# Kernel tuning notes

Hardware: AMD Instinct MI355X
Metric: run time of the kernel (lower is better)

Reference implementation:

```python
import jax, jax.numpy as jnp
import numpy as np

N_NODES = 100000


def gcn_conv(x, W, b, src, dst, n):
    # x: [N, Fin], W: [Fin, Fout]. GCNConv: D^-1/2 (A+I) D^-1/2 (X W) + b
    h = x @ W  # [N, Fout]
    ones = jnp.ones_like(dst, dtype=h.dtype)
    deg = jax.ops.segment_sum(ones, dst, num_segments=n)  # in-degree incl self-loops
    dinv = jnp.where(deg > 0, jax.lax.rsqrt(deg), 0.0)
    norm = dinv[src] * dinv[dst]  # [E]
    msg = h[src] * norm[:, None]  # gather + scale
    out = jax.ops.segment_sum(msg, dst, num_segments=n)  # scatter-add
    return out + b


def setup_inputs() -> dict:
    key = jax.random.key(0)
    k1, k2, k3, k4 = jax.random.split(key, 4)
    F_IN, H, C, E = 512, 256, 40, 3200000
    x = jax.random.normal(k1, (N_NODES, F_IN), dtype=jnp.float32)
    # glorot-ish init
    W1 = jax.random.normal(k2, (F_IN, H), dtype=jnp.float32) * (1.0 / np.sqrt(F_IN))
    b1 = jnp.zeros((H,), dtype=jnp.float32)
    W2 = jax.random.normal(k3, (H, C), dtype=jnp.float32) * (1.0 / np.sqrt(H))
    b2 = jnp.zeros((C,), dtype=jnp.float32)
    edge_index = jax.random.randint(k4, (2, E), 0, N_NODES, dtype=jnp.int64)
    return {"x": x, "W1": W1, "b1": b1, "W2": W2, "b2": b2, "edge_index": edge_index}


def reference(x, W1, b1, W2, b2, edge_index):
    n = x.shape[0]
    # add self-loops (PyG GCNConv default add_self_loops=True)
    loop = jnp.arange(n, dtype=edge_index.dtype)
    src = jnp.concatenate([edge_index[0], loop])
    dst = jnp.concatenate([edge_index[1], loop])
    h = gcn_conv(x, W1, b1, src, dst, n)
    h = jax.nn.relu(h)
    # F.dropout(training=self.training): identity in eval mode
    h = gcn_conv(h, W2, b2, src, dst, n)
    return jax.nn.log_softmax(h, axis=1)
```

## Files before the change

kernel.cpp:

```cpp
#include <hip/hip_runtime.h>
#include <stdint.h>

typedef __attribute__((ext_vector_type(8))) short bf16x8;
typedef __attribute__((ext_vector_type(4))) float f32x4;
typedef __attribute__((ext_vector_type(4))) int i32x4;

__device__ __forceinline__ unsigned short f2bf(float f) {
    unsigned int u = __float_as_uint(f);
    u += 0x7FFFu + ((u >> 16) & 1u);
    return (unsigned short)(u >> 16);
}
__device__ __forceinline__ float bf2f(unsigned short s) {
    return __uint_as_float(((unsigned int)s) << 16);
}
__device__ __forceinline__ unsigned char fp8_enc(float f) {
    f = fminf(fmaxf(f, -448.f), 448.f);
    unsigned int u = __float_as_uint(f * 0x1p-120f);
    u += 0x7FFFFu + ((u >> 20) & 1u);
    return (unsigned char)(((u >> 20) & 0x7F) | ((u >> 24) & 0x80));
}

#define SLAB_CAP 5120

__global__ __launch_bounds__(256) void k_bscatter(const int* __restrict__ src,
                                                  const int* __restrict__ dst, int E,
                                                  int* __restrict__ bcnt,
                                                  int* __restrict__ slab, int nbuck) {
    __shared__ int lh[1024];
    __shared__ int lcur[1024];
    const int CH = 8192;
    int e0 = blockIdx.x * CH;
    int e1 = min(E, e0 + CH);
    for (int i = threadIdx.x; i < nbuck; i += 256) lh[i] = 0;
    __syncthreads();
    for (int i = e0 + threadIdx.x; i < e1; i += 256) atomicAdd(&lh[dst[i] >> 7], 1);
    __syncthreads();
    for (int i = threadIdx.x; i < nbuck; i += 256) {
        int c = lh[i];
        lh[i] = c ? atomicAdd(&bcnt[i], c) : 0;
        lcur[i] = 0;
    }
    __syncthreads();
    for (int i = e0 + threadIdx.x; i < e1; i += 256) {
        int d = dst[i], s = src[i];
        int b = d >> 7;
        int p = lh[b] + atomicAdd(&lcur[b], 1);
        if (p < SLAB_CAP) slab[(size_t)b * SLAB_CAP + p] = ((d & 127) << 20) | s;
    }
}

__global__ __launch_bounds__(1024) void k_bscan(const int* __restrict__ bcnt,
                                                int* __restrict__ bbase, int nbuck) {
    __shared__ int sh[1024];
    int t = threadIdx.x;
    int v = (t < nbuck) ? min(bcnt[t], SLAB_CAP) : 0;
    sh[t] = v;
    __syncthreads();
    for (int off = 1; off < 1024; off <<= 1) {
        int x = (t >= off) ? sh[t - off] : 0;
        __syncthreads();
        sh[t] += x;
        __syncthreads();
    }
    if (t < nbuck) bbase[t] = sh[t] - v;
    if (t == 1023) bbase[nbuck] = sh[1023];
}

__global__ __launch_bounds__(256) void k_bcsr(const int* __restrict__ slab,
                                              const int* __restrict__ bcnt,
                                              const int* __restrict__ bbase,
                                              int* __restrict__ rowp,
                                              int* __restrict__ col,
                                              float* __restrict__ dinv, int n, int nbuck) {
    __shared__ int lh[128], lsc[128], lcur[128];
    const int b = blockIdx.x;
    const int base = bbase[b];
    const int cnt = min(bcnt[b], SLAB_CAP);
    const int t = threadIdx.x;
    const int* sl = slab + (size_t)b * SLAB_CAP;
    if (t < 128) lh[t] = 0;
    __syncthreads();
    for (int i = t; i < cnt; i += 256) atomicAdd(&lh[sl[i] >> 20], 1);
    __syncthreads();
    if (t < 128) lsc[t] = lh[t];
    __syncthreads();
    for (int off = 1; off < 128; off <<= 1) {
        int x = (t < 128 && t >= off) ? lsc[t - off] : 0;
        __syncthreads();
        if (t < 128) lsc[t] += x;
        __syncthreads();
    }
    if (t < 128) {
        int excl = lsc[t] - lh[t];
        lcur[t] = excl;
        int v = (b << 7) + t;
        if (v < n) {
            rowp[v] = base + excl;
            dinv[v] = rsqrtf((float)lh[t] + 1.0f);
        }
    }
    if (b == 0 && t == 0) rowp[n] = bbase[nbuck];
    __syncthreads();
    for (int i = t; i < cnt; i += 256) {
        int pk = sl[i];
        int d = pk >> 20;
        int p = base + atomicAdd(&lcur[d], 1);
        col[p] = pk & 0xFFFFF;
    }
}

__global__ __launch_bounds__(256) void k_cvt_w(const float* __restrict__ W1,
                                               const float* __restrict__ W2,
                                               short* __restrict__ W1t,
                                               short* __restrict__ W2t,
                                               int n1, int n2) {
    int i = blockIdx.x * blockDim.x + threadIdx.x;
    if (i < n1) {
        int k = i >> 8, c = i & 255;
        W1t[(size_t)c * 512 + k] = (short)f2bf(W1[i]);
    } else if (i < n1 + n2) {
        int i2 = i - n1;
        int k = i2 / 40, c = i2 - k * 40;
        W2t[(size_t)c * 256 + k] = (short)f2bf(W2[i2]);
    }
}

__global__ __launch_bounds__(512) void k_gemm1(const float* __restrict__ A,
                                               const short* __restrict__ Bt,
                                               const float* __restrict__ dinv,
                                               unsigned char* __restrict__ outp, int M) {
    const int K = 512;
    __shared__ __align__(16) short As[128 * 32];
    __shared__ __align__(16) short Bs[256 * 32];
    const int tid = threadIdx.x;
    const int m0 = blockIdx.x * 128;
    const int w = tid >> 6, lane = tid & 63;
    const int quad = lane >> 4, l16 = lane & 15;
    const int mbase = (w >> 2) * 64, nbase = (w & 3) * 64;

    f32x4 acc[4][4];
#pragma unroll
    for (int i = 0; i < 4; i++)
#pragma unroll
        for (int j = 0; j < 4; j++) acc[i][j] = (f32x4){0.f, 0.f, 0.f, 0.f};

    for (int k0 = 0; k0 < K; k0 += 32) {
#pragma unroll
        for (int s = tid; s < 1024; s += 512) {
            int r = s >> 3, seg = s & 7;
            int gr = m0 + r;
            if (gr >= M) gr = M - 1;
            float4 v = *(const float4*)(A + (size_t)gr * K + k0 + seg * 4);
            ushort4 o;
            o.x = f2bf(v.x); o.y = f2bf(v.y); o.z = f2bf(v.z); o.w = f2bf(v.w);
            *(ushort4*)(As + r * 32 + seg * 4) = o;
        }
#pragma unroll
        for (int s = tid; s < 1024; s += 512) {
            int r = s >> 2, seg = s & 3;
            i32x4 v = *(const i32x4*)(Bt + (size_t)r * K + k0 + seg * 8);
            *(i32x4*)(Bs + r * 32 + seg * 8) = v;
        }
        __syncthreads();
        bf16x8 af[4], bfr[4];
#pragma unroll
        for (int i = 0; i < 4; i++)
            af[i] = *(const bf16x8*)(As + (mbase + i * 16 + l16) * 32 + quad * 8);
#pragma unroll
        for (int j = 0; j < 4; j++)
            bfr[j] = *(const bf16x8*)(Bs + (nbase + j * 16 + l16) * 32 + quad * 8);
#pragma unroll
        for (int i = 0; i < 4; i++)
#pragma unroll
            for (int j = 0; j < 4; j++)
                acc[i][j] = __builtin_amdgcn_mfma_f32_16x16x32_bf16(af[i], bfr[j], acc[i][j], 0, 0, 0);
        __syncthreads();
    }

#pragma unroll
    for (int i = 0; i < 4; i++) {
#pragma unroll
        for (int r = 0; r < 4; r++) {
            int row = m0 + mbase + i * 16 + quad * 4 + r;
            if (row < M) {
                float dv = dinv[row] * 64.f;
#pragma unroll
                for (int j = 0; j < 4; j++)
                    outp[(size_t)row * 256 + nbase + j * 16 + l16] =
                        fp8_enc(acc[i][j][r] * dv);
            }
        }
    }
}

template <int NJ>
__global__ __launch_bounds__(256) void k_gemm_bt(const short* __restrict__ A,
                                                 const short* __restrict__ Bt,
                                                 const float* __restrict__ dinv,
                                                 short* __restrict__ outp,
                                                 int M, int K, int ldo, int ncols) {
    constexpr int BN = 32 * NJ;
    __shared__ __align__(16) short As[128 * 32];
    __shared__ __align__(16) short Bs[BN * 32];
    const int tid = threadIdx.x;
    const int m0 = blockIdx.x * 128;
    const int n0 = blockIdx.y * BN;
    const int w = tid >> 6, lane = tid & 63;
    const int quad = lane >> 4, l16 = lane & 15;
    const int mbase = (w >> 1) * 64, nbase = (w & 1) * (NJ * 16);

    f32x4 acc[4][NJ];
#pragma unroll
    for (int i = 0; i < 4; i++)
#pragma unroll
        for (int j = 0; j < NJ; j++) acc[i][j] = (f32x4){0.f, 0.f, 0.f, 0.f};

    for (int k0 = 0; k0 < K; k0 += 32) {
#pragma unroll
        for (int s = tid; s < 512; s += 256) {
            int r = s >> 2, seg = s & 3;
            int gr = m0 + r;
            if (gr >= M) gr = M - 1;
            i32x4 v = *(const i32x4*)(A + (size_t)gr * K + k0 + seg * 8);
            *(i32x4*)(As + r * 32 + seg * 8) = v;
        }
#pragma unroll
        for (int s = tid; s < BN * 4; s += 256) {
            int r = s >> 2, seg = s & 3;
            i32x4 v = *(const i32x4*)(Bt + (size_t)(n0 + r) * K + k0 + seg * 8);
            *(i32x4*)(Bs + r * 32 + seg * 8) = v;
        }
        __syncthreads();
        bf16x8 af[4], bfr[NJ];
#pragma unroll
        for (int i = 0; i < 4; i++)
            af[i] = *(const bf16x8*)(As + (mbase + i * 16 + l16) * 32 + quad * 8);
#pragma unroll
        for (int j = 0; j < NJ; j++)
            bfr[j] = *(const bf16x8*)(Bs + (nbase + j * 16 + l16) * 32 + quad * 8);
#pragma unroll
        for (int i = 0; i < 4; i++)
#pragma unroll
            for (int j = 0; j < NJ; j++)
                acc[i][j] = __builtin_amdgcn_mfma_f32_16x16x32_bf16(af[i], bfr[j], acc[i][j], 0, 0, 0);
        __syncthreads();
    }

#pragma unroll
    for (int i = 0; i < 4; i++) {
#pragma unroll
        for (int r = 0; r < 4; r++) {
            int row = m0 + mbase + i * 16 + quad * 4 + r;
            if (row < M) {
                float dv = dinv[row];
#pragma unroll
                for (int j = 0; j < NJ; j++) {
                    int c = n0 + nbase + j * 16 + l16;
                    if (c < ncols)
                        outp[(size_t)row * ldo + c] = (short)f2bf(acc[i][j][r] * dv);
                }
            }
        }
    }
}

__global__ __launch_bounds__(256) void k_agg1(const unsigned char* __restrict__ h1p,
                                              const int* __restrict__ rowp,
                                              const int* __restrict__ col,
                                              const float* __restrict__ dinv,
                                              const float* __restrict__ b1,
                                              short* __restrict__ h2, int n) {
    const unsigned int* __restrict__ hw = (const unsigned int*)h1p;
    const int w = threadIdx.x >> 6, lane = threadIdx.x & 63;
    const int v = blockIdx.x * 4 + w;
    if (v >= n) return;
    float a0, a1, a2, a3;
    {
        unsigned int u = hw[(size_t)v * 64 + lane];
        a0 = __builtin_amdgcn_cvt_f32_fp8(u, 0);
        a1 = __builtin_amdgcn_cvt_f32_fp8(u, 1);
        a2 = __builtin_amdgcn_cvt_f32_fp8(u, 2);
        a3 = __builtin_amdgcn_cvt_f32_fp8(u, 3);
    }
    const int e0 = rowp[v], e1 = rowp[v + 1];
    int e = e0;
    for (; e + 4 <= e1; e += 4) {
        int s0 = col[e], s1 = col[e + 1], s2 = col[e + 2], s3 = col[e + 3];
        unsigned int u0 = hw[(size_t)s0 * 64 + lane];
        unsigned int u1 = hw[(size_t)s1 * 64 + lane];
        unsigned int u2 = hw[(size_t)s2 * 64 + lane];
        unsigned int u3 = hw[(size_t)s3 * 64 + lane];
        a0 += __builtin_amdgcn_cvt_f32_fp8(u0, 0) + __builtin_amdgcn_cvt_f32_fp8(u1, 0)
            + __builtin_amdgcn_cvt_f32_fp8(u2, 0) + __builtin_amdgcn_cvt_f32_fp8(u3, 0);
        a1 += __builtin_amdgcn_cvt_f32_fp8(u0, 1) + __builtin_amdgcn_cvt_f32_fp8(u1, 1)
            + __builtin_amdgcn_cvt_f32_fp8(u2, 1) + __builtin_amdgcn_cvt_f32_fp8(u3, 1);
        a2 += __builtin_amdgcn_cvt_f32_fp8(u0, 2) + __builtin_amdgcn_cvt_f32_fp8(u1, 2)
            + __builtin_amdgcn_cvt_f32_fp8(u2, 2) + __builtin_amdgcn_cvt_f32_fp8(u3, 2);
        a3 += __builtin_amdgcn_cvt_f32_fp8(u0, 3) + __builtin_amdgcn_cvt_f32_fp8(u1, 3)
            + __builtin_amdgcn_cvt_f32_fp8(u2, 3) + __builtin_amdgcn_cvt_f32_fp8(u3, 3);
    }
    for (; e < e1; e++) {
        unsigned int u = hw[(size_t)col[e] * 64 + lane];
        a0 += __builtin_amdgcn_cvt_f32_fp8(u, 0);
        a1 += __builtin_amdgcn_cvt_f32_fp8(u, 1);
        a2 += __builtin_amdgcn_cvt_f32_fp8(u, 2);
        a3 += __builtin_amdgcn_cvt_f32_fp8(u, 3);
    }
    const int c4 = lane * 4;
    const float dv = dinv[v] * 0x1p-6f;
    float r0 = fmaxf(fmaf(dv, a0, b1[c4 + 0]), 0.f);
    float r1 = fmaxf(fmaf(dv, a1, b1[c4 + 1]), 0.f);
    float r2 = fmaxf(fmaf(dv, a2, b1[c4 + 2]), 0.f);
    float r3 = fmaxf(fmaf(dv, a3, b1[c4 + 3]), 0.f);
    ushort4 o;
    o.x = f2bf(r0); o.y = f2bf(r1); o.z = f2bf(r2); o.w = f2bf(r3);
    *(ushort4*)(h2 + (size_t)v * 256 + c4) = o;
}

__global__ __launch_bounds__(256) void k_agg2(const short* __restrict__ zp,
                                              const int* __restrict__ rowp,
                                              const int* __restrict__ col,
                                              const float* __restrict__ dinv,
                                              const float* __restrict__ b2,
                                              float* __restrict__ out, int n) {
    const int w = threadIdx.x >> 6, lane = threadIdx.x & 63;
    const int v = blockIdx.x * 4 + w;
    if (v >= n) return;
    const bool act = lane < 40;
    const int li = act ? lane : 0;
    float acc = act ? bf2f((unsigned short)zp[(size_t)v * 40 + li]) : 0.f;
    const int e0 = rowp[v], e1 = rowp[v + 1];
    int e = e0;
    for (; e + 4 <= e1; e += 4) {
        int sa = col[e], sb = col[e + 1], sc = col[e + 2], sd = col[e + 3];
        float fa = bf2f((unsigned short)zp[(size_t)sa * 40 + li]);
        float fb = bf2f((unsigned short)zp[(size_t)sb * 40 + li]);
        float fc = bf2f((unsigned short)zp[(size_t)sc * 40 + li]);
        float fd = bf2f((unsigned short)zp[(size_t)sd * 40 + li]);
        if (act) acc += fa + fb + fc + fd;
    }
    for (; e < e1; e++) {
        float f = bf2f((unsigned short)zp[(size_t)col[e] * 40 + li]);
        if (act) acc += f;
    }
    float logit = act ? fmaf(dinv[v], acc, b2[li]) : -1e30f;
    float m = logit;
    for (int off = 32; off; off >>= 1) m = fmaxf(m, __shfl_xor(m, off));
    float ex = act ? expf(logit - m) : 0.f;
    float ssum = ex;
    for (int off = 32; off; off >>= 1) ssum += __shfl_xor(ssum, off);
    if (act) out[(size_t)v * 40 + lane] = logit - m - logf(ssum);
}

extern "C" void kernel_launch(void* const* d_in, const int* in_sizes, int n_in,
                              void* d_out, int out_size, void* d_ws, size_t ws_size,
                              hipStream_t stream) {
    const float* x  = (const float*)d_in[0];
    const float* W1 = (const float*)d_in[1];
    const float* b1 = (const float*)d_in[2];
    const float* W2 = (const float*)d_in[3];
    const float* b2 = (const float*)d_in[4];
    const int*   ei = (const int*)d_in[5];
    float* out = (float*)d_out;

    const int FIN = 512, H = 256, C = 40;
    const int n = in_sizes[0] / FIN;
    const int E = in_sizes[5] / 2;
    const int nbuck = (n + 127) >> 7;

    auto align_up = [](size_t v) { return (v + 255) & ~(size_t)255; };
    char* base = (char*)d_ws;
    size_t off = 0;
    unsigned char* h1p = (unsigned char*)(base + off); off += align_up((size_t)n * H);
    short* h2    = (short*)(base + off); off += align_up((size_t)n * H * 2);
    short* zp    = (short*)(base + off); off += align_up((size_t)n * C * 2);
    float* dinv  = (float*)(base + off); off += align_up((size_t)n * 4);
    int* rowp    = (int*)(base + off);   off += align_up((size_t)(n + 1) * 4);
    int* colarr  = (int*)(base + off);   off += align_up((size_t)E * 4);
    int* slab    = (int*)(base + off);   off += align_up((size_t)nbuck * SLAB_CAP * 4);
    short* W1t   = (short*)(base + off); off += align_up((size_t)H * FIN * 2);
    short* W2t   = (short*)(base + off); off += align_up((size_t)64 * H * 2);
    int* bcnt    = (int*)(base + off);   off += align_up((size_t)(nbuck + 1) * 4);
    int* bbase   = (int*)(base + off);   off += align_up((size_t)(nbuck + 1) * 4);

    const int* srcp = ei;
    const int* dstp = ei + E;

    hipMemsetAsync(bcnt, 0, (size_t)(nbuck + 1) * 4, stream);
    hipMemsetAsync(W2t, 0, (size_t)64 * H * 2, stream);

    k_bscatter<<<(E + 8191) / 8192, 256, 0, stream>>>(srcp, dstp, E, bcnt, slab, nbuck);
    k_bscan<<<1, 1024, 0, stream>>>(bcnt, bbase, nbuck);
    k_bcsr<<<nbuck, 256, 0, stream>>>(slab, bcnt, bbase, rowp, colarr, dinv, n, nbuck);

    int n1 = FIN * H, n2 = H * C;
    k_cvt_w<<<(n1 + n2 + 255) / 256, 256, 0, stream>>>(W1, W2, W1t, W2t, n1, n2);

    k_gemm1<<<(n + 127) / 128, 512, 0, stream>>>(x, W1t, dinv, h1p, n);
    k_agg1<<<(n + 3) / 4, 256, 0, stream>>>(h1p, rowp, colarr, dinv, b1, h2, n);

    dim3 g2((n + 127) / 128, 1);
    k_gemm_bt<2><<<g2, 256, 0, stream>>>(h2, W2t, dinv, zp, n, H, C, C);
    k_agg2<<<(n + 3) / 4, 256, 0, stream>>>(zp, rowp, colarr, dinv, b2, out, n);
}
```

Baseline: 702.2 us.

## Store layer-2 features as scaled fp8 and aggregate four nodes per wavefront

The second GEMM now writes dinv-scaled features as fp8 (times 64) in a 64-byte padded row instead of 40 bf16 values. The layer-2 aggregation reads them as 32-bit words. Each 16-lane group handles one node with four features per lane, so a wavefront covers four nodes instead of one node with 24 idle lanes. This targets the cost of the random gather in the second aggregation and the wasted lanes, at the price of lower precision in the layer-2 messages.

```diff
diff --git a/kernel.cpp b/kernel.cpp
--- a/kernel.cpp
+++ b/kernel.cpp
@@ -193,27 +193,24 @@
     }
 }
 
-template <int NJ>
-__global__ __launch_bounds__(256) void k_gemm_bt(const short* __restrict__ A,
-                                                 const short* __restrict__ Bt,
-                                                 const float* __restrict__ dinv,
-                                                 short* __restrict__ outp,
-                                                 int M, int K, int ldo, int ncols) {
-    constexpr int BN = 32 * NJ;
+__global__ __launch_bounds__(256) void k_gemm2(const short* __restrict__ A,
+                                               const short* __restrict__ Bt,
+                                               const float* __restrict__ dinv,
+                                               unsigned char* __restrict__ outp, int M) {
+    const int K = 256;
     __shared__ __align__(16) short As[128 * 32];
-    __shared__ __align__(16) short Bs[BN * 32];
+    __shared__ __align__(16) short Bs[64 * 32];
     const int tid = threadIdx.x;
     const int m0 = blockIdx.x * 128;
-    const int n0 = blockIdx.y * BN;
     const int w = tid >> 6, lane = tid & 63;
     const int quad = lane >> 4, l16 = lane & 15;
-    const int mbase = (w >> 1) * 64, nbase = (w & 1) * (NJ * 16);
-
-    f32x4 acc[4][NJ];
+    const int mbase = (w >> 1) * 64, nbase = (w & 1) * 32;
+
+    f32x4 acc[4][2];
 #pragma unroll
     for (int i = 0; i < 4; i++)
 #pragma unroll
-        for (int j = 0; j < NJ; j++) acc[i][j] = (f32x4){0.f, 0.f, 0.f, 0.f};
+        for (int j = 0; j < 2; j++) acc[i][j] = (f32x4){0.f, 0.f, 0.f, 0.f};
 
     for (int k0 = 0; k0 < K; k0 += 32) {
 #pragma unroll
@@ -224,24 +221,23 @@
             i32x4 v = *(const i32x4*)(A + (size_t)gr * K + k0 + seg * 8);
             *(i32x4*)(As + r * 32 + seg * 8) = v;
         }
-#pragma unroll
-        for (int s = tid; s < BN * 4; s += 256) {
-            int r = s >> 2, seg = s & 3;
-            i32x4 v = *(const i32x4*)(Bt + (size_t)(n0 + r) * K + k0 + seg * 8);
+        if (tid < 256) {
+            int r = tid >> 2, seg = tid & 3;
+            i32x4 v = *(const i32x4*)(Bt + (size_t)r * K + k0 + seg * 8);
             *(i32x4*)(Bs + r * 32 + seg * 8) = v;
         }
         __syncthreads();
-        bf16x8 af[4], bfr[NJ];
+        bf16x8 af[4], bfr[2];
 #pragma unroll
         for (int i = 0; i < 4; i++)
             af[i] = *(const bf16x8*)(As + (mbase + i * 16 + l16) * 32 + quad * 8);
 #pragma unroll
-        for (int j = 0; j < NJ; j++)
+        for (int j = 0; j < 2; j++)
             bfr[j] = *(const bf16x8*)(Bs + (nbase + j * 16 + l16) * 32 + quad * 8);
 #pragma unroll
         for (int i = 0; i < 4; i++)
 #pragma unroll
-            for (int j = 0; j < NJ; j++)
+            for (int j = 0; j < 2; j++)
                 acc[i][j] = __builtin_amdgcn_mfma_f32_16x16x32_bf16(af[i], bfr[j], acc[i][j], 0, 0, 0);
         __syncthreads();
     }
@@ -252,13 +248,11 @@
         for (int r = 0; r < 4; r++) {
             int row = m0 + mbase + i * 16 + quad * 4 + r;
             if (row < M) {
-                float dv = dinv[row];
-#pragma unroll
-                for (int j = 0; j < NJ; j++) {
-                    int c = n0 + nbase + j * 16 + l16;
-                    if (c < ncols)
-                        outp[(size_t)row * ldo + c] = (short)f2bf(acc[i][j][r] * dv);
-                }
+                float dv = dinv[row] * 64.f;
+#pragma unroll
+                for (int j = 0; j < 2; j++)
+                    outp[(size_t)row * 64 + nbase + j * 16 + l16] =
+                        fp8_enc(acc[i][j][r] * dv);
             }
         }
     }
@@ -317,39 +311,70 @@
     *(ushort4*)(h2 + (size_t)v * 256 + c4) = o;
 }
 
-__global__ __launch_bounds__(256) void k_agg2(const short* __restrict__ zp,
+__global__ __launch_bounds__(256) void k_agg2(const unsigned char* __restrict__ zp,
                                               const int* __restrict__ rowp,
                                               const int* __restrict__ col,
                                               const float* __restrict__ dinv,
                                               const float* __restrict__ b2,
                                               float* __restrict__ out, int n) {
+    const unsigned int* __restrict__ zw = (const unsigned int*)zp;
     const int w = threadIdx.x >> 6, lane = threadIdx.x & 63;
-    const int v = blockIdx.x * 4 + w;
+    const int g = lane >> 4, sl = lane & 15;
+    const int v = blockIdx.x * 16 + w * 4 + g;
     if (v >= n) return;
-    const bool act = lane < 40;
-    const int li = act ? lane : 0;
-    float acc = act ? bf2f((unsigned short)zp[(size_t)v * 40 + li]) : 0.f;
+    float a0, a1, a2, a3;
+    {
+        unsigned int u = zw[(size_t)v * 16 + sl];
+        a0 = __builtin_amdgcn_cvt_f32_fp8(u, 0);
+        a1 = __builtin_amdgcn_cvt_f32_fp8(u, 1);
+        a2 = __builtin_amdgcn_cvt_f32_fp8(u, 2);
+        a3 = __builtin_amdgcn_cvt_f32_fp8(u, 3);
+    }
     const int e0 = rowp[v], e1 = rowp[v + 1];
     int e = e0;
     for (; e + 4 <= e1; e += 4) {
-        int sa = col[e], sb = col[e + 1], sc = col[e + 2], sd = col[e + 3];
-        float fa = bf2f((unsigned short)zp[(size_t)sa * 40 + li]);
-        float fb = bf2f((unsigned short)zp[(size_t)sb * 40 + li]);
-        float fc = bf2f((unsigned short)zp[(size_t)sc * 40 + li]);
-        float fd = bf2f((unsigned short)zp[(size_t)sd * 40 + li]);
-        if (act) acc += fa + fb + fc + fd;
+        int s0 = col[e], s1 = col[e + 1], s2 = col[e + 2], s3 = col[e + 3];
+        unsigned int u0 = zw[(size_t)s0 * 16 + sl];
+        unsigned int u1 = zw[(size_t)s1 * 16 + sl];
+        unsigned int u2 = zw[(size_t)s2 * 16 + sl];
+        unsigned int u3 = zw[(size_t)s3 * 16 + sl];
+        a0 += __builtin_amdgcn_cvt_f32_fp8(u0, 0) + __builtin_amdgcn_cvt_f32_fp8(u1, 0)
+            + __builtin_amdgcn_cvt_f32_fp8(u2, 0) + __builtin_amdgcn_cvt_f32_fp8(u3, 0);
+        a1 += __builtin_amdgcn_cvt_f32_fp8(u0, 1) + __builtin_amdgcn_cvt_f32_fp8(u1, 1)
+            + __builtin_amdgcn_cvt_f32_fp8(u2, 1) + __builtin_amdgcn_cvt_f32_fp8(u3, 1);
+        a2 += __builtin_amdgcn_cvt_f32_fp8(u0, 2) + __builtin_amdgcn_cvt_f32_fp8(u1, 2)
+            + __builtin_amdgcn_cvt_f32_fp8(u2, 2) + __builtin_amdgcn_cvt_f32_fp8(u3, 2);
+        a3 += __builtin_amdgcn_cvt_f32_fp8(u0, 3) + __builtin_amdgcn_cvt_f32_fp8(u1, 3)
+            + __builtin_amdgcn_cvt_f32_fp8(u2, 3) + __builtin_amdgcn_cvt_f32_fp8(u3, 3);
     }
     for (; e < e1; e++) {
-        float f = bf2f((unsigned short)zp[(size_t)col[e] * 40 + li]);
-        if (act) acc += f;
-    }
-    float logit = act ? fmaf(dinv[v], acc, b2[li]) : -1e30f;
-    float m = logit;
-    for (int off = 32; off; off >>= 1) m = fmaxf(m, __shfl_xor(m, off));
-    float ex = act ? expf(logit - m) : 0.f;
-    float ssum = ex;
-    for (int off = 32; off; off >>= 1) ssum += __shfl_xor(ssum, off);
-    if (act) out[(size_t)v * 40 + lane] = logit - m - logf(ssum);
+        unsigned int u = zw[(size_t)col[e] * 16 + sl];
+        a0 += __builtin_amdgcn_cvt_f32_fp8(u, 0);
+        a1 += __builtin_amdgcn_cvt_f32_fp8(u, 1);
+        a2 += __builtin_amdgcn_cvt_f32_fp8(u, 2);
+        a3 += __builtin_amdgcn_cvt_f32_fp8(u, 3);
+    }
+    const int f = sl * 4;
+    const float dv = dinv[v] * 0x1p-6f;
+    float l0 = (f + 0 < 40) ? fmaf(dv, a0, b2[f + 0]) : -1e30f;
+    float l1 = (f + 1 < 40) ? fmaf(dv, a1, b2[f + 1]) : -1e30f;
+    float l2 = (f + 2 < 40) ? fmaf(dv, a2, b2[f + 2]) : -1e30f;
+    float l3 = (f + 3 < 40) ? fmaf(dv, a3, b2[f + 3]) : -1e30f;
+    float m = fmaxf(fmaxf(l0, l1), fmaxf(l2, l3));
+    m = fmaxf(m, __shfl_xor(m, 1));
+    m = fmaxf(m, __shfl_xor(m, 2));
+    m = fmaxf(m, __shfl_xor(m, 4));
+    m = fmaxf(m, __shfl_xor(m, 8));
+    float es = expf(l0 - m) + expf(l1 - m) + expf(l2 - m) + expf(l3 - m);
+    es += __shfl_xor(es, 1);
+    es += __shfl_xor(es, 2);
+    es += __shfl_xor(es, 4);
+    es += __shfl_xor(es, 8);
+    float ls = m + logf(es);
+    if (sl < 10) {
+        float4 o = {l0 - ls, l1 - ls, l2 - ls, l3 - ls};
+        *(float4*)(out + (size_t)v * 40 + f) = o;
+    }
 }
 
 extern "C" void kernel_launch(void* const* d_in, const int* in_sizes, int n_in,
@@ -373,7 +398,7 @@
     size_t off = 0;
     unsigned char* h1p = (unsigned char*)(base + off); off += align_up((size_t)n * H);
     short* h2    = (short*)(base + off); off += align_up((size_t)n * H * 2);
-    short* zp    = (short*)(base + off); off += align_up((size_t)n * C * 2);
+    unsigned char* zp = (unsigned char*)(base + off); off += align_up((size_t)n * 64);
     float* dinv  = (float*)(base + off); off += align_up((size_t)n * 4);
     int* rowp    = (int*)(base + off);   off += align_up((size_t)(n + 1) * 4);
     int* colarr  = (int*)(base + off);   off += align_up((size_t)E * 4);
@@ -399,7 +424,6 @@
     k_gemm1<<<(n + 127) / 128, 512, 0, stream>>>(x, W1t, dinv, h1p, n);
     k_agg1<<<(n + 3) / 4, 256, 0, stream>>>(h1p, rowp, colarr, dinv, b1, h2, n);
 
-    dim3 g2((n + 127) / 128, 1);
-    k_gemm_bt<2><<<g2, 256, 0, stream>>>(h2, W2t, dinv, zp, n, H, C, C);
-    k_agg2<<<(n + 3) / 4, 256, 0, stream>>>(zp, rowp, colarr, dinv, b2, out, n);
-}
+    k_gemm2<<<(n + 127) / 128, 256, 0, stream>>>(h2, W2t, dinv, zp, n);
+    k_agg2<<<(n + 15) / 16, 256, 0, stream>>>(zp, rowp, colarr, dinv, b2, out, n);
+}
```

After: 639.2 us. 9.0% less time.
